# Performance work log

Hardware: AMD Instinct MI355X
Metric: run time of the kernel (lower is better)

## Reference

```python
import jax, jax.numpy as jnp
import numpy as np

HIDDEN = 1024
HEADS = 16
HEAD_DIM = HIDDEN // HEADS


def rotate_half(x):
    x1, x2 = jnp.split(x, 2, axis=-1)
    return jnp.concatenate([-x2, x1], axis=-1)


def rope_cos_sin(T, head_dim):
    inv_freq = 1.0 / (10000.0 ** (jnp.arange(0, head_dim, 2, dtype=jnp.float32) / head_dim))
    pos = jnp.arange(T, dtype=jnp.float32)
    freqs = jnp.einsum('i,j->ij', pos, inv_freq)          # [T, head_dim/2]
    emb = jnp.concatenate([freqs, freqs], axis=-1)        # [T, head_dim]
    # broadcast shape [1, T, 1, head_dim]
    return jnp.cos(emb)[None, :, None, :], jnp.sin(emb)[None, :, None, :]


def setup_inputs() -> dict:
    key = jax.random.key(0)
    ks = jax.random.split(key, 9)
    B, T = 4, 2048
    s = 1.0 / np.sqrt(HIDDEN)
    x = jax.random.normal(ks[0], (B, T, HIDDEN), dtype=jnp.float32)
    Wq = jax.random.uniform(ks[1], (HIDDEN, HIDDEN), minval=-s, maxval=s, dtype=jnp.float32)
    bq = jax.random.uniform(ks[2], (HIDDEN,), minval=-s, maxval=s, dtype=jnp.float32)
    Wk = jax.random.uniform(ks[3], (HIDDEN, HIDDEN), minval=-s, maxval=s, dtype=jnp.float32)
    bk = jax.random.uniform(ks[4], (HIDDEN,), minval=-s, maxval=s, dtype=jnp.float32)
    Wv = jax.random.uniform(ks[5], (HIDDEN, HIDDEN), minval=-s, maxval=s, dtype=jnp.float32)
    bv = jax.random.uniform(ks[6], (HIDDEN,), minval=-s, maxval=s, dtype=jnp.float32)
    Wo = jax.random.uniform(ks[7], (HIDDEN, HIDDEN), minval=-s, maxval=s, dtype=jnp.float32)
    bo = jax.random.uniform(ks[8], (HIDDEN,), minval=-s, maxval=s, dtype=jnp.float32)
    return {"x": x, "Wq": Wq, "bq": bq, "Wk": Wk, "bk": bk,
            "Wv": Wv, "bv": bv, "Wo": Wo, "bo": bo}


def reference(x, Wq, bq, Wk, bk, Wv, bv, Wo, bo):
    B, T, _ = x.shape
    q = (x @ Wq + bq).reshape(B, T, HEADS, HEAD_DIM)
    k = (x @ Wk + bk).reshape(B, T, HEADS, HEAD_DIM)
    v = (x @ Wv + bv).reshape(B, T, HEADS, HEAD_DIM)
    cos, sin = rope_cos_sin(T, HEAD_DIM)
    q = q * cos + rotate_half(q) * sin
    k = k * cos + rotate_half(k) * sin
    scale = jnp.sqrt(jnp.float32(HEAD_DIM))
    scores = jnp.einsum('bqhd,bkhd->bhqk', q, k) / scale   # [B,H,T,T]
    causal = jnp.tril(jnp.ones((T, T), dtype=bool))
    scores = jnp.where(causal[None, None], scores, -jnp.inf)
    probs = jax.nn.softmax(scores, axis=-1)
    attn = jnp.einsum('bhqk,bkhd->bqhd', probs, v).reshape(B, T, HIDDEN)
    return attn @ Wo + bo
```

## Files before the change

kernel.cpp:

```cpp
#include <hip/hip_runtime.h>

typedef unsigned short u16;
typedef __attribute__((ext_vector_type(4))) float f32x4;
typedef __attribute__((ext_vector_type(16))) float f32x16;
typedef __attribute__((ext_vector_type(8))) short s16x8;

#define B_   4
#define T_   2048
#define H_   16
#define D_   64
#define HID  1024
#define BT   (B_*T_)
#define N3   3072

__device__ inline u16 f2b(float f) {
  union { float f; unsigned u; } v; v.f = f;
  unsigned u = v.u;
  unsigned r = (u + 0x7FFFu + ((u >> 16) & 1u)) >> 16;
  return (u16)r;
}

__device__ inline void gll16(const u16* g, u16* l) {
  __builtin_amdgcn_global_load_lds(
      (const __attribute__((address_space(1))) unsigned int*)g,
      (__attribute__((address_space(3))) unsigned int*)l, 16, 0, 0);
}

__device__ inline int swz8(int row) { return (row ^ (row >> 3)) & 7; }

__global__ void k_cast4(const float* __restrict__ src, u16* __restrict__ dst, int n4) {
  int i = blockIdx.x * blockDim.x + threadIdx.x;
  if (i >= n4) return;
  float4 v = ((const float4*)src)[i];
  ushort4 o;
  o.x = f2b(v.x); o.y = f2b(v.y); o.z = f2b(v.z); o.w = f2b(v.w);
  ((ushort4*)dst)[i] = o;
}

__global__ void k_ropetab(float2* __restrict__ tab) {
  int i = blockIdx.x * blockDim.x + threadIdx.x;
  int d = i & 31, t = i >> 5;
  float inv = expf(-0.28782313662425574f * (float)d);
  float ang = (float)t * inv;
  float c, s;
  sincosf(ang, &s, &c);
  tab[i] = make_float2(c, s);
}

__global__ __launch_bounds__(256) void k_packT(const float* __restrict__ W0,
                                               const float* __restrict__ W1,
                                               const float* __restrict__ W2,
                                               u16* __restrict__ Wt) {
  __shared__ float L[64][68];
  int n0 = blockIdx.x * 64, k0 = blockIdx.y * 64;
  int which = n0 >> 10;
  const float* W = (which == 0) ? W0 : (which == 1) ? W1 : W2;
  int nc = n0 & 1023;
  int tid = threadIdx.x;
  #pragma unroll
  for (int i = 0; i < 4; i++) {
    int ch = tid + 256 * i;
    int kr = ch >> 4, cc = ch & 15;
    float4 v = *(const float4*)(W + (size_t)(k0 + kr) * 1024 + nc + cc * 4);
    *(float4*)(&L[kr][cc * 4]) = v;
  }
  __syncthreads();
  #pragma unroll
  for (int i = 0; i < 2; i++) {
    int ch = tid + 256 * i;
    int nr = ch >> 3, ck = ch & 7;
    u16 tmp[8];
    #pragma unroll
    for (int j = 0; j < 8; j++) tmp[j] = f2b(L[ck * 8 + j][nr]);
    *(uint4*)(Wt + (size_t)(n0 + nr) * 1024 + k0 + ck * 8) = *(uint4*)tmp;
  }
}

template<int MODE>
__global__ __launch_bounds__(256) void gemm_k(
    const u16* __restrict__ A, const u16* __restrict__ Bt,
    const float* __restrict__ b0, const float* __restrict__ b1,
    const float* __restrict__ b2, const float2* __restrict__ tab,
    void* __restrict__ outp, int N, int K)
{
  __shared__ __align__(16) char SM[34816];
  u16* As = (u16*)SM;
  u16* Bs = (u16*)(SM + 16384);
  int tid = threadIdx.x, lane = tid & 63, w = tid >> 6;
  int l15 = lane & 15, g = lane >> 4;
  int wm = (w >> 1) * 64, wn = (w & 1) * 64;
  int mbase = blockIdx.y * 128, nbase = blockIdx.x * 128;
  f32x4 acc[4][4] = {};

  auto STAGE = [&](int bufi, int k0) {
    #pragma unroll
    for (int i = 0; i < 2; i++) {
      int f = i * 256 + tid;
      int row = f >> 2, c = f & 3;
      gll16(A  + (size_t)(mbase + row) * K + k0 + c * 8, &As[bufi * 4096 + f * 8]);
      gll16(Bt + (size_t)(nbase + row) * K + k0 + c * 8, &Bs[bufi * 4096 + f * 8]);
    }
  };

  STAGE(0, 0);
  int cur = 0;
  for (int k0 = 0; k0 < K; k0 += 32) {
    __syncthreads();
    if (k0 + 32 < K) STAGE(cur ^ 1, k0 + 32);
    s16x8 af[4], bf[4];
    #pragma unroll
    for (int mt = 0; mt < 4; mt++)
      af[mt] = *(const s16x8*)(&As[cur * 4096 + (wm + mt * 16 + l15) * 32 + g * 8]);
    #pragma unroll
    for (int nt = 0; nt < 4; nt++)
      bf[nt] = *(const s16x8*)(&Bs[cur * 4096 + (wn + nt * 16 + l15) * 32 + g * 8]);
    #pragma unroll
    for (int mt = 0; mt < 4; mt++)
      #pragma unroll
      for (int nt = 0; nt < 4; nt++)
        acc[mt][nt] = __builtin_amdgcn_mfma_f32_16x16x32_bf16(af[mt], bf[nt], acc[mt][nt], 0, 0, 0);
    cur ^= 1;
  }

  if (MODE == 0) {
    int which = nbase >> 10;
    const float* bp = (which == 0) ? b0 : (which == 1) ? b1 : b2;
    u16* Lt = (u16*)SM;
    __syncthreads();
    if (which < 2) {
      const float FSC = (which == 0) ? 0.18033688011112043f : 1.0f;
      #pragma unroll
      for (int mt = 0; mt < 4; mt++) {
        #pragma unroll
        for (int r = 0; r < 4; r++) {
          int ml = wm + mt * 16 + g * 4 + r;
          int t = (mbase + ml) & (T_ - 1);
          #pragma unroll
          for (int nt = 0; nt < 2; nt++) {
            int nl = wn + nt * 16 + l15;
            int gn = nbase + nl;
            float2 cs = tab[t * 32 + (nl & 63)];
            float a0 = acc[mt][nt][r]     + bp[gn & 1023];
            float a1 = acc[mt][nt + 2][r] + bp[(gn + 32) & 1023];
            Lt[ml * 136 + nl]      = f2b((a0 * cs.x - a1 * cs.y) * FSC);
            Lt[ml * 136 + nl + 32] = f2b((a1 * cs.x + a0 * cs.y) * FSC);
          }
        }
      }
      __syncthreads();
      #pragma unroll
      for (int i = 0; i < 8; i++) {
        int c = tid + 256 * i;
        int row = c >> 4, cc = c & 15;
        int gm = mbase + row;
        int t = gm & (T_ - 1), bb = gm >> 11;
        int gn0 = nbase + cc * 8;
        int h = (gn0 >> 6) & (H_ - 1), d0 = gn0 & 63;
        uint4 v = *(const uint4*)(Lt + row * 136 + cc * 8);
        *(uint4*)((u16*)outp + ((size_t)((which * B_ + bb) * H_ + h) * T_ + t) * D_ + d0) = v;
      }
    } else {
      #pragma unroll
      for (int mt = 0; mt < 4; mt++)
        #pragma unroll
        for (int nt = 0; nt < 4; nt++) {
          int nl = wn + nt * 16 + l15;
          float bias = bp[(nbase + nl) & 1023];
          u16 t4[4];
          #pragma unroll
          for (int r = 0; r < 4; r++) t4[r] = f2b(acc[mt][nt][r] + bias);
          *(uint2*)(Lt + nl * 136 + wm + mt * 16 + g * 4) = *(uint2*)t4;
        }
      __syncthreads();
      #pragma unroll
      for (int i = 0; i < 8; i++) {
        int c = tid + 256 * i;
        int row = c >> 4, cc = c & 15;
        int gn = nbase + row;
        int h = (gn >> 6) & (H_ - 1), d = gn & 63;
        int m0 = mbase + cc * 8;
        int bb = m0 >> 11, t0 = m0 & (T_ - 1);
        uint4 v = *(const uint4*)(Lt + row * 136 + cc * 8);
        *(uint4*)((u16*)outp + ((size_t)((2 * B_ + bb) * H_ + h) * D_ + d) * T_ + t0) = v;
      }
    }
  } else {
    #pragma unroll
    for (int mt = 0; mt < 4; mt++)
      #pragma unroll
      for (int nt = 0; nt < 4; nt++)
        #pragma unroll
        for (int r = 0; r < 4; r++) {
          int gm = mbase + wm + mt * 16 + g * 4 + r;
          int gn = nbase + wn + nt * 16 + l15;
          ((float*)outp)[(size_t)gm * N + gn] = acc[mt][nt][r] + b0[gn];
        }
  }
}

__global__ __launch_bounds__(512, 4) void k_flash(const u16* __restrict__ Qh,
                                                  const u16* __restrict__ Kh,
                                                  const u16* __restrict__ Vtg,
                                                  u16* __restrict__ O) {
  __shared__ __align__(16) char smem[65536];
  const int tid = threadIdx.x;
  const int lane = tid & 63;
  const int l31 = lane & 31, hi = lane >> 5;
  const int w = tid >> 6, grp = w >> 2, wi = w & 3;
  const int tidg = tid & 255;
  const int bh = blockIdx.x, p = blockIdx.y;
  const int b = bh >> 4, h = bh & 15;
  const size_t hb = (size_t)bh * T_ * D_;

  u16* kbase = (u16*)(smem + grp * 32768);

  const int f0 = tidg, f1 = 256 + tidg;
  const int r0 = f0 >> 3, c0 = (f0 & 7) ^ swz8(r0);
  const int r1 = f1 >> 3, c1 = (f1 & 7) ^ swz8(r1);
  const u16* kg0 = Kh + hb + (size_t)r0 * 64 + c0 * 8;
  const u16* kg1 = Kh + hb + (size_t)r1 * 64 + c1 * 8;
  const u16* vg0 = Vtg + hb + (size_t)r0 * T_ + c0 * 8;
  const u16* vg1 = Vtg + hb + (size_t)r1 * T_ + c1 * 8;

  auto STAGE = [&](int bufi, int kvblk) {
    u16* kb = kbase + bufi * 8192;
    int kv0 = kvblk * 64;
    gll16(kg0 + (size_t)kv0 * 64, kb + f0 * 8);
    gll16(kg1 + (size_t)kv0 * 64, kb + f1 * 8);
    gll16(vg0 + kv0, kb + 4096 + f0 * 8);
    gll16(vg1 + kv0, kb + 4096 + f1 * 8);
  };

  const int sw = (grp == 1) ? (2 * p + 2) : 17;
  int tile = (grp == 1) ? p : (15 - p);

  s16x8 qf[4];
  auto LOADQ = [&](int tl) {
    const u16* qp = Qh + hb + (size_t)(tl * 128 + wi * 32 + l31) * 64 + hi * 8;
    #pragma unroll
    for (int kc = 0; kc < 4; kc++) qf[kc] = *(const s16x8*)(qp + kc * 16);
  };
  LOADQ(tile);

  f32x16 o0 = {}, o1 = {};
  float l_ = 0.f;

  auto EPI = [&](int tl) {
    float inv = 1.0f / l_;
    int q = tl * 128 + wi * 32 + l31;
    size_t ob = ((size_t)b * T_ + q) * HID + h * 64 + hi * 4;
    #pragma unroll
    for (int k = 0; k < 4; k++) {
      u16 t4[4];
      #pragma unroll
      for (int j = 0; j < 4; j++) t4[j] = f2b(o0[k * 4 + j] * inv);
      *(uint2*)(O + ob + k * 8) = *(uint2*)t4;
      #pragma unroll
      for (int j = 0; j < 4; j++) t4[j] = f2b(o1[k * 4 + j] * inv);
      *(uint2*)(O + ob + 32 + k * 8) = *(uint2*)t4;
    }
  };

  STAGE(0, 0);
  for (int i = 0; i < 17; i++) {
    __syncthreads();
    if (i + 1 < 17) {
      int nb = (i + 1 < sw) ? (i + 1) : (17 + (i + 1) - sw);
      STAGE((i + 1) & 1, nb);
    }
    if (grp == 1 && i == sw) {
      EPI(tile);
      f32x16 z = {};
      o0 = z; o1 = z; l_ = 0.f;
      tile = 15 - p;
      LOADQ(tile);
    }
    int kvblk = (i < sw) ? i : (17 + i - sw);
    int kv0 = kvblk * 64;
    int qw0 = tile * 128 + wi * 32;
    if (kv0 > qw0 + 31) continue;

    const char* Kb = (const char*)kbase + (i & 1) * 16384;
    const char* Vb = Kb + 8192;

    f32x16 S0 = {}, S1 = {};
    const int swzl = swz8(l31) << 4, swzh = swz8(32 + l31) << 4;
    __builtin_amdgcn_s_setprio(1);
    #pragma unroll
    for (int kc = 0; kc < 4; kc++) {
      s16x8 kf0 = *(const s16x8*)(Kb + ((l31 * 128 + kc * 32 + hi * 16) ^ swzl));
      s16x8 kf1 = *(const s16x8*)(Kb + (((32 + l31) * 128 + kc * 32 + hi * 16) ^ swzh));
      S0 = __builtin_amdgcn_mfma_f32_32x32x16_bf16(kf0, qf[kc], S0, 0, 0, 0);
      S1 = __builtin_amdgcn_mfma_f32_32x32x16_bf16(kf1, qf[kc], S1, 0, 0, 0);
    }
    __builtin_amdgcn_s_setprio(0);

    if (kv0 + 63 > qw0) {
      int qrel = qw0 + l31 - kv0 - 4 * hi;
      #pragma unroll
      for (int r = 0; r < 16; r++) {
        const int kvr = (r & 3) + 8 * (r >> 2);
        if (kvr > qrel)      S0[r] = -__builtin_inff();
        if (kvr + 32 > qrel) S1[r] = -__builtin_inff();
      }
    }

    float rs = 0.f;
    __builtin_amdgcn_s_setprio(1);
    #pragma unroll
    for (int h2 = 0; h2 < 2; h2++) {
      #pragma unroll
      for (int cc = 0; cc < 2; cc++) {
        float e[8];
        #pragma unroll
        for (int j = 0; j < 8; j++) {
          int r = cc * 8 + j;
          e[j] = __builtin_exp2f(h2 ? S1[r] : S0[r]);
          rs += e[j];
        }
        unsigned p0, p1, p2, p3;
        asm("v_cvt_pk_bf16_f32 %0, %1, %2" : "=v"(p0) : "v"(e[0]), "v"(e[1]));
        asm("v_cvt_pk_bf16_f32 %0, %1, %2" : "=v"(p1) : "v"(e[2]), "v"(e[3]));
        asm("v_cvt_pk_bf16_f32 %0, %1, %2" : "=v"(p2) : "v"(e[4]), "v"(e[5]));
        asm("v_cvt_pk_bf16_f32 %0, %1, %2" : "=v"(p3) : "v"(e[6]), "v"(e[7]));
        asm("v_permlane32_swap_b32 %0, %1" : "+v"(p0), "+v"(p2));
        asm("v_permlane32_swap_b32 %0, %1" : "+v"(p1), "+v"(p3));
        union { unsigned u[4]; s16x8 v; } pb;
        pb.u[0] = p0; pb.u[1] = p1; pb.u[2] = p2; pb.u[3] = p3;
        const int kk = h2 * 2 + cc;
        s16x8 vf0 = *(const s16x8*)(Vb + ((l31 * 128 + kk * 32 + hi * 16) ^ swzl));
        s16x8 vf1 = *(const s16x8*)(Vb + (((32 + l31) * 128 + kk * 32 + hi * 16) ^ swzh));
        o0 = __builtin_amdgcn_mfma_f32_32x32x16_bf16(vf0, pb.v, o0, 0, 0, 0);
        o1 = __builtin_amdgcn_mfma_f32_32x32x16_bf16(vf1, pb.v, o1, 0, 0, 0);
      }
    }
    __builtin_amdgcn_s_setprio(0);
    rs += __shfl_xor(rs, 32);
    l_ += rs;
  }

  __syncthreads();
  float* mb = (float*)smem;
  if (grp == 1) {
    float* rrow = mb + (wi * 64 + lane) * 36;
    #pragma unroll
    for (int k = 0; k < 4; k++) {
      f32x4 v0, v1;
      #pragma unroll
      for (int j = 0; j < 4; j++) { v0[j] = o0[k * 4 + j]; v1[j] = o1[k * 4 + j]; }
      *(f32x4*)(rrow + k * 4) = v0;
      *(f32x4*)(rrow + 16 + k * 4) = v1;
    }
    rrow[32] = l_;
  }
  __syncthreads();
  if (grp == 0) {
    float* rrow = mb + (wi * 64 + lane) * 36;
    l_ += rrow[32];
    #pragma unroll
    for (int k = 0; k < 4; k++) {
      f32x4 v0 = *(const f32x4*)(rrow + k * 4);
      f32x4 v1 = *(const f32x4*)(rrow + 16 + k * 4);
      #pragma unroll
      for (int j = 0; j < 4; j++) {
        o0[k * 4 + j] += v0[j];
        o1[k * 4 + j] += v1[j];
      }
    }
    EPI(15 - p);
  }
}

extern "C" void kernel_launch(void* const* d_in, const int* in_sizes, int n_in,
                              void* d_out, int out_size, void* d_ws, size_t ws_size,
                              hipStream_t stream) {
  const float* x  = (const float*)d_in[0];
  const float* Wq = (const float*)d_in[1];
  const float* bq = (const float*)d_in[2];
  const float* Wk = (const float*)d_in[3];
  const float* bk = (const float*)d_in[4];
  const float* Wv = (const float*)d_in[5];
  const float* bv = (const float*)d_in[6];
  const float* Wo = (const float*)d_in[7];
  const float* bo = (const float*)d_in[8];
  float* out = (float*)d_out;

  char* ws = (char*)d_ws;
  u16* xb    = (u16*)(ws);
  u16* WqkvT = (u16*)(ws + (size_t)16777216);
  u16* WoT   = (u16*)(ws + (size_t)16777216 + 6291456);
  u16* QKVh  = (u16*)(ws + (size_t)16777216 + 6291456 + 2097152);
  u16* Oattn = xb;
  float2* tab = (float2*)WoT;

  k_cast4<<<(BT * HID / 4 + 255) / 256, 256, 0, stream>>>(x, xb, BT * HID / 4);
  k_packT<<<dim3(N3 / 64, HID / 64), 256, 0, stream>>>(Wq, Wk, Wv, WqkvT);
  k_ropetab<<<256, 256, 0, stream>>>(tab);

  gemm_k<0><<<dim3(N3 / 128, BT / 128), 256, 0, stream>>>(
      xb, WqkvT, bq, bk, bv, tab, (void*)QKVh, N3, HID);

  k_packT<<<dim3(HID / 64, HID / 64), 256, 0, stream>>>(Wo, Wo, Wo, WoT);

  k_flash<<<dim3(B_ * H_, 8), 512, 0, stream>>>(
      QKVh, QKVh + (size_t)BT * HID, QKVh + 2 * (size_t)BT * HID, Oattn);

  gemm_k<1><<<dim3(HID / 128, BT / 128), 256, 0, stream>>>(
      Oattn, WoT, bo, bo, bo, nullptr, (void*)out, HID, HID);
}
```

Baseline: 183.9 us.

## Replace QKV projection GEMM with 256x256-tile, triple-buffered, swizzled 512-thread kernel

The QKV projection moves to a new kernel with 256x256 output tiles, 8 waves, a three-stage LDS ring fed by global_load_lds, an XOR swizzle on the LDS column chunks, split-phase MFMA with s_setprio, and explicit vmcnt waits. The larger tile raises arithmetic intensity and the deeper pipeline aims to hide global load latency. The old gemm_k is reduced to the output-projection path only. The trade-off is 132 KB of LDS per block (one block per CU) and only 12x32 blocks, which may leave some CUs idle.

```diff
diff --git a/kernel.cpp b/kernel.cpp
--- a/kernel.cpp
+++ b/kernel.cpp
@@ -12,6 +12,8 @@
 #define HID  1024
 #define BT   (B_*T_)
 #define N3   3072
+
+#define BARRIER() do { asm volatile("" ::: "memory"); __builtin_amdgcn_s_barrier(); asm volatile("" ::: "memory"); } while (0)
 
 __device__ inline u16 f2b(float f) {
   union { float f; unsigned u; } v; v.f = f;
@@ -76,16 +78,159 @@
   }
 }
 
+__global__ __launch_bounds__(512) void gemm256(
+    const u16* __restrict__ A, const u16* __restrict__ Bt,
+    const float* __restrict__ b0, const float* __restrict__ b1,
+    const float* __restrict__ b2, const float2* __restrict__ tab,
+    u16* __restrict__ outp)
+{
+  __shared__ __align__(16) char SM[135168];
+  const int tid = threadIdx.x, lane = tid & 63, w = tid >> 6;
+  const int l15 = lane & 15, g = lane >> 4;
+  const int wm = (w >> 2) * 128, wn = (w & 3) * 64;
+  const int mbase = blockIdx.y * 256, nbase = blockIdx.x * 256;
+  const int K = 1024, NT = 32;
+  f32x4 acc[8][4] = {};
+
+  auto SA = [&](int buf, int t) {
+    u16* dst = (u16*)(SM + buf * 32768);
+    #pragma unroll
+    for (int i = 0; i < 2; i++) {
+      int f = w * 128 + i * 64 + lane;
+      int row = f >> 2, c = (f & 3) ^ (row & 3);
+      gll16(A + (size_t)(mbase + row) * K + t * 32 + c * 8, dst + f * 8);
+    }
+  };
+  auto SB = [&](int buf, int t) {
+    u16* dst = (u16*)(SM + buf * 32768 + 16384);
+    #pragma unroll
+    for (int i = 0; i < 2; i++) {
+      int f = w * 128 + i * 64 + lane;
+      int row = f >> 2, c = (f & 3) ^ (row & 3);
+      gll16(Bt + (size_t)(nbase + row) * K + t * 32 + c * 8, dst + f * 8);
+    }
+  };
+
+  SA(0, 0); SB(0, 0); SA(1, 1); SB(1, 1);
+  asm volatile("s_waitcnt vmcnt(4)" ::: "memory");
+  BARRIER();
+
+  int cur = 0;
+  for (int t = 0; t < NT; t++) {
+    int nx = cur + 2; if (nx >= 3) nx -= 3;
+    const char* Ab = SM + cur * 32768;
+    const char* Bb = SM + cur * 32768 + 16384;
+    bool st = (t + 2 < NT);
+
+    s16x8 af[8], bf[4];
+    #pragma unroll
+    for (int mt = 0; mt < 8; mt++) {
+      int row = wm + mt * 16 + l15;
+      af[mt] = *(const s16x8*)(Ab + row * 64 + (g ^ (row & 3)) * 16);
+    }
+    #pragma unroll
+    for (int nt = 0; nt < 2; nt++) {
+      int row = wn + nt * 16 + l15;
+      bf[nt] = *(const s16x8*)(Bb + row * 64 + (g ^ (row & 3)) * 16);
+    }
+    if (st) SA(nx, t + 2);
+    BARRIER();
+    __builtin_amdgcn_s_setprio(1);
+    #pragma unroll
+    for (int mt = 0; mt < 8; mt++) {
+      acc[mt][0] = __builtin_amdgcn_mfma_f32_16x16x32_bf16(af[mt], bf[0], acc[mt][0], 0, 0, 0);
+      acc[mt][1] = __builtin_amdgcn_mfma_f32_16x16x32_bf16(af[mt], bf[1], acc[mt][1], 0, 0, 0);
+    }
+    __builtin_amdgcn_s_setprio(0);
+    BARRIER();
+
+    #pragma unroll
+    for (int nt = 2; nt < 4; nt++) {
+      int row = wn + nt * 16 + l15;
+      bf[nt] = *(const s16x8*)(Bb + row * 64 + (g ^ (row & 3)) * 16);
+    }
+    if (st) SB(nx, t + 2);
+    BARRIER();
+    __builtin_amdgcn_s_setprio(1);
+    #pragma unroll
+    for (int mt = 0; mt < 8; mt++) {
+      acc[mt][2] = __builtin_amdgcn_mfma_f32_16x16x32_bf16(af[mt], bf[2], acc[mt][2], 0, 0, 0);
+      acc[mt][3] = __builtin_amdgcn_mfma_f32_16x16x32_bf16(af[mt], bf[3], acc[mt][3], 0, 0, 0);
+    }
+    __builtin_amdgcn_s_setprio(0);
+    if (t + 1 < NT) {
+      if (st) asm volatile("s_waitcnt vmcnt(4)" ::: "memory");
+      else    asm volatile("s_waitcnt vmcnt(0)" ::: "memory");
+    }
+    BARRIER();
+    cur = (cur == 2) ? 0 : cur + 1;
+  }
+
+  int which = nbase >> 10;
+  const float* bp = (which == 0) ? b0 : (which == 1) ? b1 : b2;
+  u16* Lt = (u16*)SM;
+  if (which < 2) {
+    const float FSC = (which == 0) ? 0.18033688011112043f : 1.0f;
+    #pragma unroll
+    for (int mt = 0; mt < 8; mt++) {
+      #pragma unroll
+      for (int r = 0; r < 4; r++) {
+        int ml = wm + mt * 16 + g * 4 + r;
+        int t = (mbase + ml) & (T_ - 1);
+        #pragma unroll
+        for (int nt = 0; nt < 2; nt++) {
+          int d = nt * 16 + l15;
+          float2 cs = tab[t * 32 + d];
+          float a0 = acc[mt][nt][r]     + bp[(nbase + wn + d) & 1023];
+          float a1 = acc[mt][nt + 2][r] + bp[(nbase + wn + d + 32) & 1023];
+          Lt[ml * 264 + wn + d]      = f2b((a0 * cs.x - a1 * cs.y) * FSC);
+          Lt[ml * 264 + wn + d + 32] = f2b((a1 * cs.x + a0 * cs.y) * FSC);
+        }
+      }
+    }
+    __syncthreads();
+    #pragma unroll
+    for (int i = 0; i < 16; i++) {
+      int c = tid + 512 * i;
+      int row = c >> 5, cc = c & 31;
+      int gm = mbase + row, t = gm & (T_ - 1), bb = gm >> 11;
+      int gn0 = nbase + cc * 8, h = (gn0 >> 6) & 15, d0 = gn0 & 63;
+      *(uint4*)(outp + ((size_t)((which * B_ + bb) * H_ + h) * T_ + t) * D_ + d0) =
+          *(const uint4*)(Lt + row * 264 + cc * 8);
+    }
+  } else {
+    #pragma unroll
+    for (int mt = 0; mt < 8; mt++) {
+      #pragma unroll
+      for (int nt = 0; nt < 4; nt++) {
+        int nl = wn + nt * 16 + l15;
+        float bias = bp[(nbase + nl) & 1023];
+        u16 t4[4];
+        #pragma unroll
+        for (int r = 0; r < 4; r++) t4[r] = f2b(acc[mt][nt][r] + bias);
+        *(uint2*)(Lt + nl * 264 + wm + mt * 16 + g * 4) = *(uint2*)t4;
+      }
+    }
+    __syncthreads();
+    #pragma unroll
+    for (int i = 0; i < 16; i++) {
+      int c = tid + 512 * i;
+      int row = c >> 5, cc = c & 31;
+      int gn = nbase + row, h = (gn >> 6) & 15, d = gn & 63;
+      int m0 = mbase + cc * 8, bb = m0 >> 11, t0 = m0 & (T_ - 1);
+      *(uint4*)(outp + ((size_t)((2 * B_ + bb) * H_ + h) * D_ + d) * T_ + t0) =
+          *(const uint4*)(Lt + row * 264 + cc * 8);
+    }
+  }
+}
+
 template<int MODE>
 __global__ __launch_bounds__(256) void gemm_k(
     const u16* __restrict__ A, const u16* __restrict__ Bt,
-    const float* __restrict__ b0, const float* __restrict__ b1,
-    const float* __restrict__ b2, const float2* __restrict__ tab,
-    void* __restrict__ outp, int N, int K)
+    const float* __restrict__ b0, void* __restrict__ outp, int N, int K)
 {
-  __shared__ __align__(16) char SM[34816];
-  u16* As = (u16*)SM;
-  u16* Bs = (u16*)(SM + 16384);
+  __shared__ __align__(16) u16 As[2][128 * 32];
+  __shared__ __align__(16) u16 Bs[2][128 * 32];
   int tid = threadIdx.x, lane = tid & 63, w = tid >> 6;
   int l15 = lane & 15, g = lane >> 4;
   int wm = (w >> 1) * 64, wn = (w & 1) * 64;
@@ -97,8 +242,8 @@
     for (int i = 0; i < 2; i++) {
       int f = i * 256 + tid;
       int row = f >> 2, c = f & 3;
-      gll16(A  + (size_t)(mbase + row) * K + k0 + c * 8, &As[bufi * 4096 + f * 8]);
-      gll16(Bt + (size_t)(nbase + row) * K + k0 + c * 8, &Bs[bufi * 4096 + f * 8]);
+      gll16(A  + (size_t)(mbase + row) * K + k0 + c * 8, &As[bufi][f * 8]);
+      gll16(Bt + (size_t)(nbase + row) * K + k0 + c * 8, &Bs[bufi][f * 8]);
     }
   };
 
@@ -110,10 +255,10 @@
     s16x8 af[4], bf[4];
     #pragma unroll
     for (int mt = 0; mt < 4; mt++)
-      af[mt] = *(const s16x8*)(&As[cur * 4096 + (wm + mt * 16 + l15) * 32 + g * 8]);
+      af[mt] = *(const s16x8*)(&As[cur][(wm + mt * 16 + l15) * 32 + g * 8]);
     #pragma unroll
     for (int nt = 0; nt < 4; nt++)
-      bf[nt] = *(const s16x8*)(&Bs[cur * 4096 + (wn + nt * 16 + l15) * 32 + g * 8]);
+      bf[nt] = *(const s16x8*)(&Bs[cur][(wn + nt * 16 + l15) * 32 + g * 8]);
     #pragma unroll
     for (int mt = 0; mt < 4; mt++)
       #pragma unroll
@@ -122,80 +267,16 @@
     cur ^= 1;
   }
 
-  if (MODE == 0) {
-    int which = nbase >> 10;
-    const float* bp = (which == 0) ? b0 : (which == 1) ? b1 : b2;
-    u16* Lt = (u16*)SM;
-    __syncthreads();
-    if (which < 2) {
-      const float FSC = (which == 0) ? 0.18033688011112043f : 1.0f;
-      #pragma unroll
-      for (int mt = 0; mt < 4; mt++) {
-        #pragma unroll
-        for (int r = 0; r < 4; r++) {
-          int ml = wm + mt * 16 + g * 4 + r;
-          int t = (mbase + ml) & (T_ - 1);
-          #pragma unroll
-          for (int nt = 0; nt < 2; nt++) {
-            int nl = wn + nt * 16 + l15;
-            int gn = nbase + nl;
-            float2 cs = tab[t * 32 + (nl & 63)];
-            float a0 = acc[mt][nt][r]     + bp[gn & 1023];
-            float a1 = acc[mt][nt + 2][r] + bp[(gn + 32) & 1023];
-            Lt[ml * 136 + nl]      = f2b((a0 * cs.x - a1 * cs.y) * FSC);
-            Lt[ml * 136 + nl + 32] = f2b((a1 * cs.x + a0 * cs.y) * FSC);
-          }
-        }
-      }
-      __syncthreads();
-      #pragma unroll
-      for (int i = 0; i < 8; i++) {
-        int c = tid + 256 * i;
-        int row = c >> 4, cc = c & 15;
-        int gm = mbase + row;
-        int t = gm & (T_ - 1), bb = gm >> 11;
-        int gn0 = nbase + cc * 8;
-        int h = (gn0 >> 6) & (H_ - 1), d0 = gn0 & 63;
-        uint4 v = *(const uint4*)(Lt + row * 136 + cc * 8);
-        *(uint4*)((u16*)outp + ((size_t)((which * B_ + bb) * H_ + h) * T_ + t) * D_ + d0) = v;
-      }
-    } else {
-      #pragma unroll
-      for (int mt = 0; mt < 4; mt++)
-        #pragma unroll
-        for (int nt = 0; nt < 4; nt++) {
-          int nl = wn + nt * 16 + l15;
-          float bias = bp[(nbase + nl) & 1023];
-          u16 t4[4];
-          #pragma unroll
-          for (int r = 0; r < 4; r++) t4[r] = f2b(acc[mt][nt][r] + bias);
-          *(uint2*)(Lt + nl * 136 + wm + mt * 16 + g * 4) = *(uint2*)t4;
-        }
-      __syncthreads();
-      #pragma unroll
-      for (int i = 0; i < 8; i++) {
-        int c = tid + 256 * i;
-        int row = c >> 4, cc = c & 15;
-        int gn = nbase + row;
-        int h = (gn >> 6) & (H_ - 1), d = gn & 63;
-        int m0 = mbase + cc * 8;
-        int bb = m0 >> 11, t0 = m0 & (T_ - 1);
-        uint4 v = *(const uint4*)(Lt + row * 136 + cc * 8);
-        *(uint4*)((u16*)outp + ((size_t)((2 * B_ + bb) * H_ + h) * D_ + d) * T_ + t0) = v;
-      }
-    }
-  } else {
-    #pragma unroll
-    for (int mt = 0; mt < 4; mt++)
-      #pragma unroll
-      for (int nt = 0; nt < 4; nt++)
-        #pragma unroll
-        for (int r = 0; r < 4; r++) {
-          int gm = mbase + wm + mt * 16 + g * 4 + r;
-          int gn = nbase + wn + nt * 16 + l15;
-          ((float*)outp)[(size_t)gm * N + gn] = acc[mt][nt][r] + b0[gn];
-        }
-  }
+  #pragma unroll
+  for (int mt = 0; mt < 4; mt++)
+    #pragma unroll
+    for (int nt = 0; nt < 4; nt++)
+      #pragma unroll
+      for (int r = 0; r < 4; r++) {
+        int gm = mbase + wm + mt * 16 + g * 4 + r;
+        int gn = nbase + wn + nt * 16 + l15;
+        ((float*)outp)[(size_t)gm * N + gn] = acc[mt][nt][r] + b0[gn];
+      }
 }
 
 __global__ __launch_bounds__(512, 4) void k_flash(const u16* __restrict__ Qh,
@@ -397,8 +478,8 @@
   k_packT<<<dim3(N3 / 64, HID / 64), 256, 0, stream>>>(Wq, Wk, Wv, WqkvT);
   k_ropetab<<<256, 256, 0, stream>>>(tab);
 
-  gemm_k<0><<<dim3(N3 / 128, BT / 128), 256, 0, stream>>>(
-      xb, WqkvT, bq, bk, bv, tab, (void*)QKVh, N3, HID);
+  gemm256<<<dim3(N3 / 256, BT / 256), 512, 0, stream>>>(
+      xb, WqkvT, bq, bk, bv, tab, QKVh);
 
   k_packT<<<dim3(HID / 64, HID / 64), 256, 0, stream>>>(Wo, Wo, Wo, WoT);
 
@@ -406,5 +487,5 @@
       QKVh, QKVh + (size_t)BT * HID, QKVh + 2 * (size_t)BT * HID, Oattn);
 
   gemm_k<1><<<dim3(HID / 128, BT / 128), 256, 0, stream>>>(
-      Oattn, WoT, bo, bo, bo, nullptr, (void*)out, HID, HID);
-}
+      Oattn, WoT, bo, (void*)out, HID, HID);
+}
```

Result: slower. 191.7 us (+4.3%).

## Merge prep kernels into one launch and swizzle GEMM block order

Applied to the files above, without the earlier changes.

The x cast, the QKV and Wo weight transposes and the RoPE table build now run as a single multi-role k_prep kernel whose role is chosen by block index range, so three or four launches become one. If the workspace is large enough, the RoPE table gets its own region, which lets the Wo transpose join the same launch. Both GEMMs remap block indices with a grouped swizzle to improve L2 reuse of tiles, and the templated GEMM is split into two specialised kernels. The cost is a branchy kernel with uneven block roles and a fallback path that depends on workspace size.

```diff
diff --git a/kernel.cpp b/kernel.cpp
--- a/kernel.cpp
+++ b/kernel.cpp
@@ -28,23 +28,65 @@
 
 __device__ inline int swz8(int row) { return (row ^ (row >> 3)) & 7; }
 
-__global__ void k_cast4(const float* __restrict__ src, u16* __restrict__ dst, int n4) {
-  int i = blockIdx.x * blockDim.x + threadIdx.x;
-  if (i >= n4) return;
-  float4 v = ((const float4*)src)[i];
-  ushort4 o;
-  o.x = f2b(v.x); o.y = f2b(v.y); o.z = f2b(v.z); o.w = f2b(v.w);
-  ((ushort4*)dst)[i] = o;
-}
-
-__global__ void k_ropetab(float2* __restrict__ tab) {
-  int i = blockIdx.x * blockDim.x + threadIdx.x;
-  int d = i & 31, t = i >> 5;
-  float inv = expf(-0.28782313662425574f * (float)d);
-  float ang = (float)t * inv;
-  float c, s;
-  sincosf(ang, &s, &c);
-  tab[i] = make_float2(c, s);
+__device__ void packT_body(float (*L)[68], const float* __restrict__ W,
+                           int nc, int k0, u16* __restrict__ outRow) {
+  int tid = threadIdx.x;
+  #pragma unroll
+  for (int i = 0; i < 4; i++) {
+    int ch = tid + 256 * i;
+    int kr = ch >> 4, cc = ch & 15;
+    float4 v = *(const float4*)(W + (size_t)(k0 + kr) * 1024 + nc + cc * 4);
+    *(float4*)(&L[kr][cc * 4]) = v;
+  }
+  __syncthreads();
+  #pragma unroll
+  for (int i = 0; i < 2; i++) {
+    int ch = tid + 256 * i;
+    int nr = ch >> 3, ck = ch & 7;
+    u16 tmp[8];
+    #pragma unroll
+    for (int j = 0; j < 8; j++) tmp[j] = f2b(L[ck * 8 + j][nr]);
+    *(uint4*)(outRow + (size_t)nr * 1024 + k0 + ck * 8) = *(uint4*)tmp;
+  }
+}
+
+__global__ __launch_bounds__(256) void k_prep(
+    const float* __restrict__ x, u16* __restrict__ xb,
+    const float* __restrict__ Wq, const float* __restrict__ Wk,
+    const float* __restrict__ Wv, u16* __restrict__ WqkvT,
+    const float* __restrict__ Wo, u16* __restrict__ WoT,
+    float2* __restrict__ tab)
+{
+  __shared__ float L[64][68];
+  int bid = blockIdx.x, tid = threadIdx.x;
+  if (bid < 2048) {
+    #pragma unroll
+    for (int j = 0; j < 4; j++) {
+      int i = bid * 1024 + j * 256 + tid;
+      float4 v = ((const float4*)x)[i];
+      ushort4 o;
+      o.x = f2b(v.x); o.y = f2b(v.y); o.z = f2b(v.z); o.w = f2b(v.w);
+      ((ushort4*)xb)[i] = o;
+    }
+  } else if (bid < 2816) {
+    int idx = bid - 2048;
+    int n0 = (idx % 48) * 64, k0 = (idx / 48) * 64;
+    int which = n0 >> 10;
+    const float* W = (which == 0) ? Wq : (which == 1) ? Wk : Wv;
+    packT_body(L, W, n0 & 1023, k0, WqkvT + (size_t)n0 * 1024);
+  } else if (bid < 3072) {
+    int i = (bid - 2816) * 256 + tid;
+    int d = i & 31, t = i >> 5;
+    float inv = expf(-0.28782313662425574f * (float)d);
+    float ang = (float)t * inv;
+    float c, s;
+    sincosf(ang, &s, &c);
+    tab[i] = make_float2(c, s);
+  } else {
+    int idx = bid - 3072;
+    int n0 = (idx & 15) * 64, k0 = (idx >> 4) * 64;
+    packT_body(L, Wo, n0, k0, WoT + (size_t)n0 * 1024);
+  }
 }
 
 __global__ __launch_bounds__(256) void k_packT(const float* __restrict__ W0,
@@ -55,33 +97,14 @@
   int n0 = blockIdx.x * 64, k0 = blockIdx.y * 64;
   int which = n0 >> 10;
   const float* W = (which == 0) ? W0 : (which == 1) ? W1 : W2;
-  int nc = n0 & 1023;
-  int tid = threadIdx.x;
-  #pragma unroll
-  for (int i = 0; i < 4; i++) {
-    int ch = tid + 256 * i;
-    int kr = ch >> 4, cc = ch & 15;
-    float4 v = *(const float4*)(W + (size_t)(k0 + kr) * 1024 + nc + cc * 4);
-    *(float4*)(&L[kr][cc * 4]) = v;
-  }
-  __syncthreads();
-  #pragma unroll
-  for (int i = 0; i < 2; i++) {
-    int ch = tid + 256 * i;
-    int nr = ch >> 3, ck = ch & 7;
-    u16 tmp[8];
-    #pragma unroll
-    for (int j = 0; j < 8; j++) tmp[j] = f2b(L[ck * 8 + j][nr]);
-    *(uint4*)(Wt + (size_t)(n0 + nr) * 1024 + k0 + ck * 8) = *(uint4*)tmp;
-  }
-}
-
-template<int MODE>
-__global__ __launch_bounds__(256) void gemm_k(
+  packT_body(L, W, n0 & 1023, k0, Wt + (size_t)n0 * 1024);
+}
+
+__global__ __launch_bounds__(256) void gemm0_k(
     const u16* __restrict__ A, const u16* __restrict__ Bt,
     const float* __restrict__ b0, const float* __restrict__ b1,
     const float* __restrict__ b2, const float2* __restrict__ tab,
-    void* __restrict__ outp, int N, int K)
+    u16* __restrict__ outp)
 {
   __shared__ __align__(16) char SM[34816];
   u16* As = (u16*)SM;
@@ -89,7 +112,10 @@
   int tid = threadIdx.x, lane = tid & 63, w = tid >> 6;
   int l15 = lane & 15, g = lane >> 4;
   int wm = (w >> 1) * 64, wn = (w & 1) * 64;
-  int mbase = blockIdx.y * 128, nbase = blockIdx.x * 128;
+  int orig = blockIdx.y * 24 + blockIdx.x;
+  int swzb = (orig & 7) * 192 + (orig >> 3);
+  int mbase = (swzb / 24) * 128, nbase = (swzb % 24) * 128;
+  const int K = HID;
   f32x4 acc[4][4] = {};
 
   auto STAGE = [&](int bufi, int k0) {
@@ -122,80 +148,123 @@
     cur ^= 1;
   }
 
-  if (MODE == 0) {
-    int which = nbase >> 10;
-    const float* bp = (which == 0) ? b0 : (which == 1) ? b1 : b2;
-    u16* Lt = (u16*)SM;
+  int which = nbase >> 10;
+  const float* bp = (which == 0) ? b0 : (which == 1) ? b1 : b2;
+  u16* Lt = (u16*)SM;
+  __syncthreads();
+  if (which < 2) {
+    const float FSC = (which == 0) ? 0.18033688011112043f : 1.0f;
+    #pragma unroll
+    for (int mt = 0; mt < 4; mt++) {
+      #pragma unroll
+      for (int r = 0; r < 4; r++) {
+        int ml = wm + mt * 16 + g * 4 + r;
+        int t = (mbase + ml) & (T_ - 1);
+        #pragma unroll
+        for (int nt = 0; nt < 2; nt++) {
+          int nl = wn + nt * 16 + l15;
+          int gn = nbase + nl;
+          float2 cs = tab[t * 32 + (nl & 63)];
+          float a0 = acc[mt][nt][r]     + bp[gn & 1023];
+          float a1 = acc[mt][nt + 2][r] + bp[(gn + 32) & 1023];
+          Lt[ml * 136 + nl]      = f2b((a0 * cs.x - a1 * cs.y) * FSC);
+          Lt[ml * 136 + nl + 32] = f2b((a1 * cs.x + a0 * cs.y) * FSC);
+        }
+      }
+    }
     __syncthreads();
-    if (which < 2) {
-      const float FSC = (which == 0) ? 0.18033688011112043f : 1.0f;
-      #pragma unroll
-      for (int mt = 0; mt < 4; mt++) {
+    #pragma unroll
+    for (int i = 0; i < 8; i++) {
+      int c = tid + 256 * i;
+      int row = c >> 4, cc = c & 15;
+      int gm = mbase + row;
+      int t = gm & (T_ - 1), bb = gm >> 11;
+      int gn0 = nbase + cc * 8;
+      int h = (gn0 >> 6) & (H_ - 1), d0 = gn0 & 63;
+      uint4 v = *(const uint4*)(Lt + row * 136 + cc * 8);
+      *(uint4*)(outp + ((size_t)((which * B_ + bb) * H_ + h) * T_ + t) * D_ + d0) = v;
+    }
+  } else {
+    #pragma unroll
+    for (int mt = 0; mt < 4; mt++)
+      #pragma unroll
+      for (int nt = 0; nt < 4; nt++) {
+        int nl = wn + nt * 16 + l15;
+        float bias = bp[(nbase + nl) & 1023];
+        u16 t4[4];
         #pragma unroll
-        for (int r = 0; r < 4; r++) {
-          int ml = wm + mt * 16 + g * 4 + r;
-          int t = (mbase + ml) & (T_ - 1);
-          #pragma unroll
-          for (int nt = 0; nt < 2; nt++) {
-            int nl = wn + nt * 16 + l15;
-            int gn = nbase + nl;
-            float2 cs = tab[t * 32 + (nl & 63)];
-            float a0 = acc[mt][nt][r]     + bp[gn & 1023];
-            float a1 = acc[mt][nt + 2][r] + bp[(gn + 32) & 1023];
-            Lt[ml * 136 + nl]      = f2b((a0 * cs.x - a1 * cs.y) * FSC);
-            Lt[ml * 136 + nl + 32] = f2b((a1 * cs.x + a0 * cs.y) * FSC);
-          }
-        }
-      }
-      __syncthreads();
-      #pragma unroll
-      for (int i = 0; i < 8; i++) {
-        int c = tid + 256 * i;
-        int row = c >> 4, cc = c & 15;
-        int gm = mbase + row;
-        int t = gm & (T_ - 1), bb = gm >> 11;
-        int gn0 = nbase + cc * 8;
-        int h = (gn0 >> 6) & (H_ - 1), d0 = gn0 & 63;
-        uint4 v = *(const uint4*)(Lt + row * 136 + cc * 8);
-        *(uint4*)((u16*)outp + ((size_t)((which * B_ + bb) * H_ + h) * T_ + t) * D_ + d0) = v;
-      }
-    } else {
-      #pragma unroll
-      for (int mt = 0; mt < 4; mt++)
-        #pragma unroll
-        for (int nt = 0; nt < 4; nt++) {
-          int nl = wn + nt * 16 + l15;
-          float bias = bp[(nbase + nl) & 1023];
-          u16 t4[4];
-          #pragma unroll
-          for (int r = 0; r < 4; r++) t4[r] = f2b(acc[mt][nt][r] + bias);
-          *(uint2*)(Lt + nl * 136 + wm + mt * 16 + g * 4) = *(uint2*)t4;
-        }
-      __syncthreads();
-      #pragma unroll
-      for (int i = 0; i < 8; i++) {
-        int c = tid + 256 * i;
-        int row = c >> 4, cc = c & 15;
-        int gn = nbase + row;
-        int h = (gn >> 6) & (H_ - 1), d = gn & 63;
-        int m0 = mbase + cc * 8;
-        int bb = m0 >> 11, t0 = m0 & (T_ - 1);
-        uint4 v = *(const uint4*)(Lt + row * 136 + cc * 8);
-        *(uint4*)((u16*)outp + ((size_t)((2 * B_ + bb) * H_ + h) * D_ + d) * T_ + t0) = v;
-      }
-    }
-  } else {
+        for (int r = 0; r < 4; r++) t4[r] = f2b(acc[mt][nt][r] + bias);
+        *(uint2*)(Lt + nl * 136 + wm + mt * 16 + g * 4) = *(uint2*)t4;
+      }
+    __syncthreads();
+    #pragma unroll
+    for (int i = 0; i < 8; i++) {
+      int c = tid + 256 * i;
+      int row = c >> 4, cc = c & 15;
+      int gn = nbase + row;
+      int h = (gn >> 6) & (H_ - 1), d = gn & 63;
+      int m0 = mbase + cc * 8;
+      int bb = m0 >> 11, t0 = m0 & (T_ - 1);
+      uint4 v = *(const uint4*)(Lt + row * 136 + cc * 8);
+      *(uint4*)(outp + ((size_t)((2 * B_ + bb) * H_ + h) * D_ + d) * T_ + t0) = v;
+    }
+  }
+}
+
+__global__ __launch_bounds__(256) void gemm_k(
+    const u16* __restrict__ A, const u16* __restrict__ Bt,
+    const float* __restrict__ b0, void* __restrict__ outp, int N, int K)
+{
+  __shared__ __align__(16) u16 As[2][128 * 32];
+  __shared__ __align__(16) u16 Bs[2][128 * 32];
+  int tid = threadIdx.x, lane = tid & 63, w = tid >> 6;
+  int l15 = lane & 15, g = lane >> 4;
+  int wm = (w >> 1) * 64, wn = (w & 1) * 64;
+  int orig = blockIdx.y * 8 + blockIdx.x;
+  int swzb = (orig & 7) * 64 + (orig >> 3);
+  int mbase = (swzb >> 3) * 128, nbase = (swzb & 7) * 128;
+  f32x4 acc[4][4] = {};
+
+  auto STAGE = [&](int bufi, int k0) {
+    #pragma unroll
+    for (int i = 0; i < 2; i++) {
+      int f = i * 256 + tid;
+      int row = f >> 2, c = f & 3;
+      gll16(A  + (size_t)(mbase + row) * K + k0 + c * 8, &As[bufi][f * 8]);
+      gll16(Bt + (size_t)(nbase + row) * K + k0 + c * 8, &Bs[bufi][f * 8]);
+    }
+  };
+
+  STAGE(0, 0);
+  int cur = 0;
+  for (int k0 = 0; k0 < K; k0 += 32) {
+    __syncthreads();
+    if (k0 + 32 < K) STAGE(cur ^ 1, k0 + 32);
+    s16x8 af[4], bf[4];
     #pragma unroll
     for (int mt = 0; mt < 4; mt++)
+      af[mt] = *(const s16x8*)(&As[cur][(wm + mt * 16 + l15) * 32 + g * 8]);
+    #pragma unroll
+    for (int nt = 0; nt < 4; nt++)
+      bf[nt] = *(const s16x8*)(&Bs[cur][(wn + nt * 16 + l15) * 32 + g * 8]);
+    #pragma unroll
+    for (int mt = 0; mt < 4; mt++)
       #pragma unroll
       for (int nt = 0; nt < 4; nt++)
-        #pragma unroll
-        for (int r = 0; r < 4; r++) {
-          int gm = mbase + wm + mt * 16 + g * 4 + r;
-          int gn = nbase + wn + nt * 16 + l15;
-          ((float*)outp)[(size_t)gm * N + gn] = acc[mt][nt][r] + b0[gn];
-        }
-  }
+        acc[mt][nt] = __builtin_amdgcn_mfma_f32_16x16x32_bf16(af[mt], bf[nt], acc[mt][nt], 0, 0, 0);
+    cur ^= 1;
+  }
+
+  #pragma unroll
+  for (int mt = 0; mt < 4; mt++)
+    #pragma unroll
+    for (int nt = 0; nt < 4; nt++)
+      #pragma unroll
+      for (int r = 0; r < 4; r++) {
+        int gm = mbase + wm + mt * 16 + g * 4 + r;
+        int gn = nbase + wn + nt * 16 + l15;
+        ((float*)outp)[(size_t)gm * N + gn] = acc[mt][nt][r] + b0[gn];
+      }
 }
 
 __global__ __launch_bounds__(512, 4) void k_flash(const u16* __restrict__ Qh,
@@ -391,20 +460,23 @@
   u16* WoT   = (u16*)(ws + (size_t)16777216 + 6291456);
   u16* QKVh  = (u16*)(ws + (size_t)16777216 + 6291456 + 2097152);
   u16* Oattn = xb;
-  float2* tab = (float2*)WoT;
-
-  k_cast4<<<(BT * HID / 4 + 255) / 256, 256, 0, stream>>>(x, xb, BT * HID / 4);
-  k_packT<<<dim3(N3 / 64, HID / 64), 256, 0, stream>>>(Wq, Wk, Wv, WqkvT);
-  k_ropetab<<<256, 256, 0, stream>>>(tab);
-
-  gemm_k<0><<<dim3(N3 / 128, BT / 128), 256, 0, stream>>>(
-      xb, WqkvT, bq, bk, bv, tab, (void*)QKVh, N3, HID);
-
-  k_packT<<<dim3(HID / 64, HID / 64), 256, 0, stream>>>(Wo, Wo, Wo, WoT);
+
+  const size_t used = (size_t)16777216 + 6291456 + 2097152 + 50331648;
+  bool all4 = ws_size >= used + 524288;
+  float2* tab = all4 ? (float2*)(ws + used) : (float2*)WoT;
+
+  k_prep<<<all4 ? 3328 : 3072, 256, 0, stream>>>(
+      x, xb, Wq, Wk, Wv, WqkvT, Wo, WoT, tab);
+
+  gemm0_k<<<dim3(24, 64), 256, 0, stream>>>(
+      xb, WqkvT, bq, bk, bv, tab, QKVh);
+
+  if (!all4)
+    k_packT<<<dim3(HID / 64, HID / 64), 256, 0, stream>>>(Wo, Wo, Wo, WoT);
 
   k_flash<<<dim3(B_ * H_, 8), 512, 0, stream>>>(
       QKVh, QKVh + (size_t)BT * HID, QKVh + 2 * (size_t)BT * HID, Oattn);
 
-  gemm_k<1><<<dim3(HID / 128, BT / 128), 256, 0, stream>>>(
-      Oattn, WoT, bo, bo, bo, nullptr, (void*)out, HID, HID);
-}
+  gemm_k<<<dim3(HID / 128, BT / 128), 256, 0, stream>>>(
+      Oattn, WoT, bo, (void*)out, HID, HID);
+}
```

Result: no change. 184.1 us (+0.2%).
